# Kernel optimization log

Hardware: AMD Instinct MI355X
Metric: run time of the kernel (lower is better)

## Reference

```python
import jax, jax.numpy as jnp
import numpy as np

NUM_GRAPHS = 512

def setup_inputs() -> dict:
    key = jax.random.key(0)
    ks = jax.random.split(key, 8)
    N, E, SD = 50000, 800000, 128
    x_ids = jax.random.randint(ks[0], (N,), 0, 1340)
    edge_index = jax.random.randint(ks[1], (2, E), 0, N)
    batch = jnp.sort(jax.random.randint(ks[2], (N,), 0, NUM_GRAPHS))
    emb = jax.random.normal(ks[3], (1340, SD), dtype=jnp.float32) * 0.1
    W1 = jax.random.normal(ks[4], (SD, 2 * SD), dtype=jnp.float32) * 0.1
    b1 = jnp.zeros((2 * SD,), dtype=jnp.float32)
    W2 = jax.random.normal(ks[5], (2 * SD, 41), dtype=jnp.float32) * 0.1
    b2 = jnp.zeros((41,), dtype=jnp.float32)
    return {"x_ids": x_ids, "edge_index": edge_index, "batch": batch,
            "emb": emb, "W1": W1, "b1": b1, "W2": W2, "b2": b2}

def _gcn_conv(x, src, dst, W, b, num_nodes):
    # x: [N, Fin] -> [N, Fout]; GCN: add self-loops, deg^-1/2 norm, transform, aggregate
    deg = jax.ops.segment_sum(jnp.ones_like(dst, dtype=x.dtype), dst, num_segments=num_nodes)
    dinv = jnp.where(deg > 0, jax.lax.rsqrt(jnp.where(deg > 0, deg, 1.0)), 0.0)
    norm = dinv[src] * dinv[dst]               # [E+N]
    h = x @ W                                  # [N, Fout]
    msg = h[src] * norm[:, None]               # [E+N, Fout] gather (memory-bound)
    out = jax.ops.segment_sum(msg, dst, num_segments=num_nodes)
    return out + b

def reference(x_ids, edge_index, batch, emb, W1, b1, W2, b2):
    N = x_ids.shape[0]
    loops = jnp.arange(N, dtype=edge_index.dtype)
    src = jnp.concatenate([edge_index[0], loops])
    dst = jnp.concatenate([edge_index[1], loops])
    x = emb[x_ids]                                   # embedding lookup [N, SD]
    x = _gcn_conv(x, src, dst, W1, b1, N)
    x = jax.nn.relu(x)                               # dropout is identity in eval mode
    x = _gcn_conv(x, src, dst, W2, b2, N)
    return jax.ops.segment_sum(x, batch, num_segments=NUM_GRAPHS)  # [512, 41]
```

## Files before the change

kernel.cpp:

```cpp
#include <hip/hip_runtime.h>

#define N_NODES 50000
#define N_EDGES 800000
#define N_TOT   850000
#define SD 128
#define HD 256
#define OD 41
#define ODP 48
#define NG 512
#define NB 128
#define NPB 391
#define BCAP 8192

typedef __attribute__((ext_vector_type(8))) short bh8;
typedef __attribute__((ext_vector_type(4))) float f4;
typedef unsigned long long u64;

__device__ inline unsigned short f2bf(float x) {
  unsigned u = __float_as_uint(x);
  unsigned r = u + 0x7fff + ((u >> 16) & 1);
  return (unsigned short)(r >> 16);
}
__device__ inline float bf2f(unsigned short s) {
  return __uint_as_float(((unsigned)s) << 16);
}
__device__ inline float bflo(unsigned e) { return __uint_as_float(e << 16); }
__device__ inline float bfhi(unsigned e) { return __uint_as_float(e & 0xffff0000u); }
__device__ inline unsigned pk2(float lo, float hi) {
  return (unsigned)f2bf(lo) | ((unsigned)f2bf(hi) << 16);
}

__device__ inline unsigned rec_xid(u64 r)  { return ((unsigned)r) >> 16; }
__device__ inline unsigned rec_src(u64 r)  { return ((unsigned)r) & 0xFFFFu; }
__device__ inline float    rec_nrm(u64 r)  { return __uint_as_float((unsigned)(r >> 32) & 0xFFFF0000u); }

__global__ __launch_bounds__(256) void init_kernel(const float* __restrict__ emb,
    const float* __restrict__ W1, const float* __restrict__ W2,
    unsigned short* __restrict__ embb, unsigned short* __restrict__ w1f,
    unsigned short* __restrict__ w2f, float4* __restrict__ curB4, float4* __restrict__ out4) {
  int tid = blockIdx.x * 256 + threadIdx.x;
  if (tid < 1340 * SD) { embb[tid] = f2bf(emb[tid]); return; }
  int u = tid - 1340 * SD;
  if (u < 4096) {
    int lane = u & 63, frag = u >> 6;
    int ks = frag >> 4, cf = frag & 15;
    int col = cf * 16 + (lane & 15);
    #pragma unroll
    for (int j = 0; j < 8; ++j) {
      int k = ks * 32 + ((lane >> 4) << 3) + j;
      w1f[u * 8 + j] = f2bf(W1[k * HD + col]);
    }
    return;
  }
  u -= 4096;
  if (u < 1536) {
    int lane = u & 63, frag = u >> 6;
    int ks = frag / 3, cf = frag % 3;
    int col = cf * 16 + (lane & 15);
    #pragma unroll
    for (int j = 0; j < 8; ++j) {
      int k = ks * 32 + ((lane >> 4) << 3) + j;
      w2f[u * 8 + j] = (col < OD) ? f2bf(W2[k * OD + col]) : (unsigned short)0;
    }
    return;
  }
  u -= 1536;
  float4 z = make_float4(0.f, 0.f, 0.f, 0.f);
  if (u < 32) { curB4[u] = z; return; }
  u -= 32;
  if (u < 5248) out4[u] = z;
}

__global__ __launch_bounds__(256) void passA_kernel(const int* __restrict__ ei,
    const int* __restrict__ x_ids, int* __restrict__ curB, u64* __restrict__ stage) {
  __shared__ int lcur[NB];
  __shared__ int base[NB];
  int t = threadIdx.x;
  if (t < NB) lcur[t] = 0;
  __syncthreads();
  u64 pay[16];
  int loc[16];
  int e0 = blockIdx.x * 4096;
  #pragma unroll
  for (int j = 0; j < 16; ++j) {
    int e = e0 + j * 256 + t;
    loc[j] = -1;
    if (e < N_TOT) {
      int s, d;
      if (e < N_EDGES) { s = ei[e]; d = ei[N_EDGES + e]; }
      else             { s = d = e - N_EDGES; }
      int b = d / NPB;
      int lofs = atomicAdd(&lcur[b], 1);
      loc[j] = (b << 13) | lofs;
      pay[j] = ((u64)(unsigned)x_ids[s] << 32) | ((u64)(unsigned)d << 16) | (u64)(unsigned)s;
    }
  }
  __syncthreads();
  if (t < NB) base[t] = atomicAdd(&curB[t], lcur[t]);
  __syncthreads();
  #pragma unroll
  for (int j = 0; j < 16; ++j) {
    if (loc[j] >= 0) {
      int b = loc[j] >> 13, lofs = loc[j] & 8191;
      stage[(size_t)b * BCAP + base[b] + lofs] = pay[j];
    }
  }
}

__global__ __launch_bounds__(256) void count_kernel(const int* __restrict__ curB,
    const u64* __restrict__ stage, int* __restrict__ vcnt, float* __restrict__ dinv) {
  __shared__ int cl[NPB];
  int t = threadIdx.x, k = blockIdx.x;
  for (int l = t; l < NPB; l += 256) cl[l] = 0;
  __syncthreads();
  int nbk = curB[k];
  const u64* st = stage + (size_t)k * BCAP;
  for (int i = t; i < nbk; i += 256) {
    int d = (int)((st[i] >> 16) & 0xFFFFu);
    atomicAdd(&cl[d - k * NPB], 1);
  }
  __syncthreads();
  int n0 = k * NPB;
  int nn = (n0 + NPB <= N_NODES) ? NPB : (N_NODES - n0);
  for (int l = t; l < nn; l += 256) {
    int v = cl[l];
    vcnt[n0 + l] = v;
    dinv[n0 + l] = rsqrtf((float)v);
  }
}

__global__ __launch_bounds__(256) void scan1_kernel(const int* __restrict__ vcnt,
    int* __restrict__ off, int* __restrict__ bsum) {
  __shared__ int lds[256];
  int t = threadIdx.x;
  int i = blockIdx.x * 256 + t;
  int v = (i < N_NODES) ? vcnt[i] : 0;
  lds[t] = v;
  __syncthreads();
  for (int s = 1; s < 256; s <<= 1) {
    int add = (t >= s) ? lds[t - s] : 0;
    __syncthreads();
    lds[t] += add;
    __syncthreads();
  }
  int inc = lds[t];
  if (i < N_NODES) off[i] = inc - v;
  if (t == 255) bsum[blockIdx.x] = inc;
}

__global__ __launch_bounds__(256) void scan3g_kernel(int* __restrict__ off,
    const int* __restrict__ bsum, const int* __restrict__ batch, int* __restrict__ gstart) {
  __shared__ int lds[256];
  int t = threadIdx.x;
  int v = (t < 196) ? bsum[t] : 0;
  lds[t] = v;
  __syncthreads();
  for (int s = 1; s < 256; s <<= 1) {
    int add = (t >= s) ? lds[t - s] : 0;
    __syncthreads();
    lds[t] += add;
    __syncthreads();
  }
  int b = blockIdx.x;
  int bso = (b == 0) ? 0 : lds[b - 1];
  int i = b * 256 + t;
  if (i < N_NODES) off[i] += bso;
  if (i == 0) off[N_NODES] = N_TOT;
  if (i < N_NODES) {
    if (i == 0) {
      for (int g = 0; g <= batch[0]; ++g) gstart[g] = 0;
    } else {
      int bp = batch[i - 1], bn = batch[i];
      for (int g = bp + 1; g <= bn; ++g) gstart[g] = i;
    }
    if (i == N_NODES - 1) {
      for (int g = batch[i] + 1; g <= NG; ++g) gstart[g] = N_NODES;
    }
  }
}

__global__ __launch_bounds__(256) void passB_kernel(const int* __restrict__ curB,
    const u64* __restrict__ stage, const int* __restrict__ off,
    const float* __restrict__ dinv, u64* __restrict__ rec) {
  __shared__ int lcur[NPB];
  __shared__ int loff[NPB];
  int t = threadIdx.x, k = blockIdx.x;
  int n0 = k * NPB;
  int nn = (n0 + NPB <= N_NODES) ? NPB : (N_NODES - n0);
  for (int l = t; l < nn; l += 256) { lcur[l] = 0; loff[l] = off[n0 + l]; }
  __syncthreads();
  int nbk = curB[k];
  const u64* st = stage + (size_t)k * BCAP;
  for (int i = t; i < nbk; i += 256) {
    u64 r = st[i];
    int s   = (int)(r & 0xFFFFu);
    int d   = (int)((r >> 16) & 0xFFFFu);
    int xid = (int)((r >> 32) & 0xFFFFu);
    float nrm = dinv[s] * dinv[d];
    int ld = d - n0;
    int p = loff[ld] + atomicAdd(&lcur[ld], 1);
    rec[p] = ((u64)f2bf(nrm) << 48) | ((u64)(unsigned)xid << 16) | (u64)(unsigned)s;
  }
}

__global__ __launch_bounds__(256) void agg1w_kernel(const int* __restrict__ off,
    const u64* __restrict__ rec, const uint4* __restrict__ emb16,
    uint4* __restrict__ agg16) {
  int lane = threadIdx.x & 63;
  int node = __builtin_amdgcn_readfirstlane(blockIdx.x * 4 + (threadIdx.x >> 6));
  int beg = off[node], end = off[node + 1];
  int eslot = lane >> 4, fgrp = lane & 15;
  float a[8];
  #pragma unroll
  for (int j = 0; j < 8; ++j) a[j] = 0.f;
  int i = beg;
  for (; i + 8 <= end; i += 8) {
    u64 rA = rec[i + eslot];
    u64 rB = rec[i + 4 + eslot];
    uint4 vA = emb16[rec_xid(rA) * 16 + fgrp];
    uint4 vB = emb16[rec_xid(rB) * 16 + fgrp];
    float nA = rec_nrm(rA), nB = rec_nrm(rB);
    a[0] += nA * bflo(vA.x); a[1] += nA * bfhi(vA.x);
    a[2] += nA * bflo(vA.y); a[3] += nA * bfhi(vA.y);
    a[4] += nA * bflo(vA.z); a[5] += nA * bfhi(vA.z);
    a[6] += nA * bflo(vA.w); a[7] += nA * bfhi(vA.w);
    a[0] += nB * bflo(vB.x); a[1] += nB * bfhi(vB.x);
    a[2] += nB * bflo(vB.y); a[3] += nB * bfhi(vB.y);
    a[4] += nB * bflo(vB.z); a[5] += nB * bfhi(vB.z);
    a[6] += nB * bflo(vB.w); a[7] += nB * bfhi(vB.w);
  }
  for (; i < end; i += 4) {
    int idx = i + eslot;
    bool val = idx < end;
    u64 r = rec[val ? idx : (end - 1)];
    uint4 v = emb16[rec_xid(r) * 16 + fgrp];
    float n = val ? rec_nrm(r) : 0.f;
    a[0] += n * bflo(v.x); a[1] += n * bfhi(v.x);
    a[2] += n * bflo(v.y); a[3] += n * bfhi(v.y);
    a[4] += n * bflo(v.z); a[5] += n * bfhi(v.z);
    a[6] += n * bflo(v.w); a[7] += n * bfhi(v.w);
  }
  #pragma unroll
  for (int j = 0; j < 8; ++j) {
    a[j] += __shfl_xor(a[j], 16);
    a[j] += __shfl_xor(a[j], 32);
  }
  if (lane < 16) {
    uint4 o;
    o.x = pk2(a[0], a[1]); o.y = pk2(a[2], a[3]);
    o.z = pk2(a[4], a[5]); o.w = pk2(a[6], a[7]);
    agg16[(size_t)node * 16 + fgrp] = o;
  }
}

__global__ __launch_bounds__(256) void gemm12_mfma(const unsigned short* __restrict__ agg1,
    const bh8* __restrict__ w1f, const float* __restrict__ b1,
    const bh8* __restrict__ w2f, unsigned short* __restrict__ h2b) {
  __shared__ char raw[32768];
  int t = threadIdx.x, lane = t & 63, wave = t >> 6;
  int row0 = blockIdx.x * 64;
  #pragma unroll
  for (int k = 0; k < 4; ++k) {
    int idx = k * 256 + t;
    int r = idx >> 4, cc = idx & 15;
    int4 v = make_int4(0, 0, 0, 0);
    if (row0 + r < N_NODES)
      v = *(const int4*)((const char*)agg1 + (size_t)(row0 + r) * 256 + cc * 16);
    *(int4*)(raw + ((r * 256 + cc * 16) ^ ((r & 15) << 4))) = v;
  }
  bh8 bf1[4][4];
  #pragma unroll
  for (int cf = 0; cf < 4; ++cf)
    #pragma unroll
    for (int ks = 0; ks < 4; ++ks)
      bf1[cf][ks] = w1f[(ks * 16 + wave * 4 + cf) * 64 + lane];
  f4 acc[4][4];
  #pragma unroll
  for (int rf = 0; rf < 4; ++rf)
    #pragma unroll
    for (int cf = 0; cf < 4; ++cf)
      acc[rf][cf] = (f4){0.f, 0.f, 0.f, 0.f};
  __syncthreads();
  #pragma unroll
  for (int ks = 0; ks < 4; ++ks) {
    bh8 a[4];
    #pragma unroll
    for (int rf = 0; rf < 4; ++rf) {
      int r = rf * 16 + (lane & 15);
      int byte = (r * 256 + ks * 64 + ((lane >> 4) << 4)) ^ ((r & 15) << 4);
      a[rf] = *(const bh8*)(raw + byte);
    }
    #pragma unroll
    for (int rf = 0; rf < 4; ++rf)
      #pragma unroll
      for (int cf = 0; cf < 4; ++cf)
        acc[rf][cf] = __builtin_amdgcn_mfma_f32_16x16x32_bf16(a[rf], bf1[cf][ks], acc[rf][cf], 0, 0, 0);
  }
  __syncthreads();
  #pragma unroll
  for (int cf = 0; cf < 4; ++cf) {
    int col = wave * 64 + cf * 16 + (lane & 15);
    float bias = b1[col];
    #pragma unroll
    for (int rf = 0; rf < 4; ++rf)
      #pragma unroll
      for (int j = 0; j < 4; ++j) {
        int r = rf * 16 + ((lane >> 4) << 2) + j;
        unsigned short v = f2bf(fmaxf(acc[rf][cf][j] + bias, 0.f));
        *(unsigned short*)(raw + ((r * 512 + col * 2) ^ ((r & 15) << 4))) = v;
      }
  }
  bh8 bf2[3][8];
  #pragma unroll
  for (int cf = 0; cf < 3; ++cf)
    #pragma unroll
    for (int ks = 0; ks < 8; ++ks)
      bf2[cf][ks] = w2f[(ks * 3 + cf) * 64 + lane];
  f4 acc2[3];
  #pragma unroll
  for (int cf = 0; cf < 3; ++cf) acc2[cf] = (f4){0.f, 0.f, 0.f, 0.f};
  __syncthreads();
  int r2 = wave * 16 + (lane & 15);
  #pragma unroll
  for (int ks = 0; ks < 8; ++ks) {
    int byte = (r2 * 512 + ks * 64 + ((lane >> 4) << 4)) ^ ((r2 & 15) << 4);
    bh8 a = *(const bh8*)(raw + byte);
    #pragma unroll
    for (int cf = 0; cf < 3; ++cf)
      acc2[cf] = __builtin_amdgcn_mfma_f32_16x16x32_bf16(a, bf2[cf][ks], acc2[cf], 0, 0, 0);
  }
  #pragma unroll
  for (int cf = 0; cf < 3; ++cf) {
    int col = cf * 16 + (lane & 15);
    #pragma unroll
    for (int j = 0; j < 4; ++j) {
      int rg = row0 + wave * 16 + ((lane >> 4) << 2) + j;
      if (rg < N_NODES)
        h2b[(size_t)rg * ODP + col] = f2bf(acc2[cf][j]);
    }
  }
}

__global__ __launch_bounds__(256) void pool2_kernel(const int* __restrict__ gstart,
    const int* __restrict__ off, const u64* __restrict__ rec,
    const unsigned short* __restrict__ h2b, const float* __restrict__ b2,
    float* __restrict__ out) {
  __shared__ float red[4][60][8];
  int g = blockIdx.x >> 3, c = blockIdx.x & 7;
  int t = threadIdx.x, lane = t & 63, wv = t >> 6;
  int n0 = gstart[g], n1 = gstart[g + 1];
  int e0 = off[n0], e1 = off[n1];
  int len = e1 - e0;
  int c0 = e0 + ((len * c) >> 3);
  int c1 = e0 + ((len * (c + 1)) >> 3);
  int clen = c1 - c0;
  int w0 = c0 + ((clen * wv) >> 2);
  int w1 = c0 + ((clen * (wv + 1)) >> 2);
  bool live = lane < 60;
  int eslot = live ? lane / 6 : 0;
  int fgrp  = live ? lane - (lane / 6) * 6 : 0;
  float a[8];
  #pragma unroll
  for (int j = 0; j < 8; ++j) a[j] = 0.f;
  int i = w0;
  for (; i + 10 <= w1; i += 10) {
    u64 r = rec[i + eslot];
    uint4 v = *(const uint4*)(h2b + (size_t)rec_src(r) * ODP + fgrp * 8);
    float n = live ? rec_nrm(r) : 0.f;
    a[0] += n * bflo(v.x); a[1] += n * bfhi(v.x);
    a[2] += n * bflo(v.y); a[3] += n * bfhi(v.y);
    a[4] += n * bflo(v.z); a[5] += n * bfhi(v.z);
    a[6] += n * bflo(v.w); a[7] += n * bfhi(v.w);
  }
  if (i < w1) {
    int idx = i + eslot;
    bool val = live && idx < w1;
    u64 r = rec[val ? idx : w0];
    uint4 v = *(const uint4*)(h2b + (size_t)rec_src(r) * ODP + fgrp * 8);
    float n = val ? rec_nrm(r) : 0.f;
    a[0] += n * bflo(v.x); a[1] += n * bfhi(v.x);
    a[2] += n * bflo(v.y); a[3] += n * bfhi(v.y);
    a[4] += n * bflo(v.z); a[5] += n * bfhi(v.z);
    a[6] += n * bflo(v.w); a[7] += n * bfhi(v.w);
  }
  if (live) {
    #pragma unroll
    for (int j = 0; j < 8; ++j) red[wv][lane][j] = a[j];
  }
  __syncthreads();
  if (t < 48) {
    int fg = t >> 3, j = t & 7;
    float s = 0.f;
    #pragma unroll
    for (int w = 0; w < 4; ++w)
      #pragma unroll
      for (int e = 0; e < 10; ++e)
        s += red[w][e * 6 + fg][j];
    if (t < OD) {
      if (c == 0) s += (float)(n1 - n0) * b2[t];
      unsafeAtomicAdd(&out[g * OD + t], s);
    }
  }
}

extern "C" void kernel_launch(void* const* d_in, const int* in_sizes, int n_in,
                              void* d_out, int out_size, void* d_ws, size_t ws_size,
                              hipStream_t stream) {
  const int*   x_ids = (const int*)d_in[0];
  const int*   ei    = (const int*)d_in[1];
  const int*   batch = (const int*)d_in[2];
  const float* emb   = (const float*)d_in[3];
  const float* W1    = (const float*)d_in[4];
  const float* b1    = (const float*)d_in[5];
  const float* W2    = (const float*)d_in[6];
  const float* b2    = (const float*)d_in[7];
  float* out = (float*)d_out;
  char* ws = (char*)d_ws;

  int*            vcnt   = (int*)           (ws + 0);
  int*            curB   = (int*)           (ws + 204800);
  float*          dinv   = (float*)         (ws + 208896);
  int*            off    = (int*)           (ws + 413696);
  int*            bsum   = (int*)           (ws + 618496);
  int*            gstart = (int*)           (ws + 620544);
  unsigned short* embb   = (unsigned short*)(ws + 1048576);
  unsigned short* w1f    = (unsigned short*)(ws + 1441792);
  unsigned short* w2f    = (unsigned short*)(ws + 1507328);
  u64*            rec    = (u64*)           (ws + 2097152);
  u64*            stage  = (u64*)           (ws + 9437184);
  unsigned short* agg1   = (unsigned short*)(ws + 18874368);
  unsigned short* h2b    = (unsigned short*)(ws + 33554432);

  init_kernel <<<713, 256, 0, stream>>>(emb, W1, W2, embb, w1f, w2f,
                                        (float4*)curB, (float4*)out);
  passA_kernel<<<208, 256, 0, stream>>>(ei, x_ids, curB, stage);
  count_kernel<<<NB,  256, 0, stream>>>(curB, stage, vcnt, dinv);
  scan1_kernel<<<196, 256, 0, stream>>>(vcnt, off, bsum);
  scan3g_kernel<<<196, 256, 0, stream>>>(off, bsum, batch, gstart);
  passB_kernel<<<NB,  256, 0, stream>>>(curB, stage, off, dinv, rec);

  agg1w_kernel<<<12500, 256, 0, stream>>>(off, rec, (const uint4*)embb, (uint4*)agg1);
  gemm12_mfma <<<782,   256, 0, stream>>>(agg1, (const bh8*)w1f, b1, (const bh8*)w2f, h2b);
  pool2_kernel<<<4096,  256, 0, stream>>>(gstart, off, rec, h2b, b2, out);
}
```

Baseline: 106.0 us.

## Fuse degree count with prefix scan, move gstart into init, deepen gather unrolls

```diff
diff --git a/kernel.cpp b/kernel.cpp
--- a/kernel.cpp
+++ b/kernel.cpp
@@ -36,8 +36,10 @@
 
 __global__ __launch_bounds__(256) void init_kernel(const float* __restrict__ emb,
     const float* __restrict__ W1, const float* __restrict__ W2,
+    const int* __restrict__ batch,
     unsigned short* __restrict__ embb, unsigned short* __restrict__ w1f,
-    unsigned short* __restrict__ w2f, float4* __restrict__ curB4, float4* __restrict__ out4) {
+    unsigned short* __restrict__ w2f, float4* __restrict__ curB4,
+    float4* __restrict__ out4, int* __restrict__ gstart) {
   int tid = blockIdx.x * 256 + threadIdx.x;
   if (tid < 1340 * SD) { embb[tid] = f2bf(emb[tid]); return; }
   int u = tid - 1340 * SD;
@@ -68,7 +70,20 @@
   float4 z = make_float4(0.f, 0.f, 0.f, 0.f);
   if (u < 32) { curB4[u] = z; return; }
   u -= 32;
-  if (u < 5248) out4[u] = z;
+  if (u < 5248) { out4[u] = z; return; }
+  u -= 5248;
+  if (u < N_NODES) {
+    int i = u;
+    if (i == 0) {
+      for (int g = 0; g <= batch[0]; ++g) gstart[g] = 0;
+    } else {
+      int bp = batch[i - 1], bn = batch[i];
+      for (int g = bp + 1; g <= bn; ++g) gstart[g] = i;
+    }
+    if (i == N_NODES - 1) {
+      for (int g = batch[i] + 1; g <= NG; ++g) gstart[g] = N_NODES;
+    }
+  }
 }
 
 __global__ __launch_bounds__(256) void passA_kernel(const int* __restrict__ ei,
@@ -107,12 +122,22 @@
   }
 }
 
-__global__ __launch_bounds__(256) void count_kernel(const int* __restrict__ curB,
-    const u64* __restrict__ stage, int* __restrict__ vcnt, float* __restrict__ dinv) {
+__global__ __launch_bounds__(256) void countscan_kernel(const int* __restrict__ curB,
+    const u64* __restrict__ stage, int* __restrict__ off, float* __restrict__ dinv) {
   __shared__ int cl[NPB];
+  __shared__ int sc[512];
+  __shared__ int bs[NB];
   int t = threadIdx.x, k = blockIdx.x;
   for (int l = t; l < NPB; l += 256) cl[l] = 0;
-  __syncthreads();
+  if (t < NB) bs[t] = curB[t];
+  __syncthreads();
+  for (int s = 1; s < NB; s <<= 1) {
+    int a = (t < NB && t >= s) ? bs[t - s] : 0;
+    __syncthreads();
+    if (t < NB) bs[t] += a;
+    __syncthreads();
+  }
+  int base = (k == 0) ? 0 : bs[k - 1];
   int nbk = curB[k];
   const u64* st = stage + (size_t)k * BCAP;
   for (int i = t; i < nbk; i += 256) {
@@ -120,63 +145,24 @@
     atomicAdd(&cl[d - k * NPB], 1);
   }
   __syncthreads();
+  sc[t]       = (t < NPB)       ? cl[t]       : 0;
+  sc[t + 256] = (t + 256 < NPB) ? cl[t + 256] : 0;
+  __syncthreads();
+  for (int s = 1; s < 512; s <<= 1) {
+    int a0 = (t >= s) ? sc[t - s] : 0;
+    int a1 = (t + 256 >= s) ? sc[t + 256 - s] : 0;
+    __syncthreads();
+    sc[t] += a0; sc[t + 256] += a1;
+    __syncthreads();
+  }
   int n0 = k * NPB;
   int nn = (n0 + NPB <= N_NODES) ? NPB : (N_NODES - n0);
   for (int l = t; l < nn; l += 256) {
     int v = cl[l];
-    vcnt[n0 + l] = v;
+    off[n0 + l] = base + sc[l] - v;
     dinv[n0 + l] = rsqrtf((float)v);
   }
-}
-
-__global__ __launch_bounds__(256) void scan1_kernel(const int* __restrict__ vcnt,
-    int* __restrict__ off, int* __restrict__ bsum) {
-  __shared__ int lds[256];
-  int t = threadIdx.x;
-  int i = blockIdx.x * 256 + t;
-  int v = (i < N_NODES) ? vcnt[i] : 0;
-  lds[t] = v;
-  __syncthreads();
-  for (int s = 1; s < 256; s <<= 1) {
-    int add = (t >= s) ? lds[t - s] : 0;
-    __syncthreads();
-    lds[t] += add;
-    __syncthreads();
-  }
-  int inc = lds[t];
-  if (i < N_NODES) off[i] = inc - v;
-  if (t == 255) bsum[blockIdx.x] = inc;
-}
-
-__global__ __launch_bounds__(256) void scan3g_kernel(int* __restrict__ off,
-    const int* __restrict__ bsum, const int* __restrict__ batch, int* __restrict__ gstart) {
-  __shared__ int lds[256];
-  int t = threadIdx.x;
-  int v = (t < 196) ? bsum[t] : 0;
-  lds[t] = v;
-  __syncthreads();
-  for (int s = 1; s < 256; s <<= 1) {
-    int add = (t >= s) ? lds[t - s] : 0;
-    __syncthreads();
-    lds[t] += add;
-    __syncthreads();
-  }
-  int b = blockIdx.x;
-  int bso = (b == 0) ? 0 : lds[b - 1];
-  int i = b * 256 + t;
-  if (i < N_NODES) off[i] += bso;
-  if (i == 0) off[N_NODES] = N_TOT;
-  if (i < N_NODES) {
-    if (i == 0) {
-      for (int g = 0; g <= batch[0]; ++g) gstart[g] = 0;
-    } else {
-      int bp = batch[i - 1], bn = batch[i];
-      for (int g = bp + 1; g <= bn; ++g) gstart[g] = i;
-    }
-    if (i == N_NODES - 1) {
-      for (int g = batch[i] + 1; g <= NG; ++g) gstart[g] = N_NODES;
-    }
-  }
+  if (k == 0 && t == 0) off[N_NODES] = N_TOT;
 }
 
 __global__ __launch_bounds__(256) void passB_kernel(const int* __restrict__ curB,
@@ -214,6 +200,33 @@
   #pragma unroll
   for (int j = 0; j < 8; ++j) a[j] = 0.f;
   int i = beg;
+  for (; i + 16 <= end; i += 16) {
+    u64 r0 = rec[i + eslot];
+    u64 r1 = rec[i + 4 + eslot];
+    u64 r2 = rec[i + 8 + eslot];
+    u64 r3 = rec[i + 12 + eslot];
+    uint4 v0 = emb16[rec_xid(r0) * 16 + fgrp];
+    uint4 v1 = emb16[rec_xid(r1) * 16 + fgrp];
+    uint4 v2 = emb16[rec_xid(r2) * 16 + fgrp];
+    uint4 v3 = emb16[rec_xid(r3) * 16 + fgrp];
+    float n0 = rec_nrm(r0), n1 = rec_nrm(r1), n2 = rec_nrm(r2), n3 = rec_nrm(r3);
+    a[0] += n0 * bflo(v0.x); a[1] += n0 * bfhi(v0.x);
+    a[2] += n0 * bflo(v0.y); a[3] += n0 * bfhi(v0.y);
+    a[4] += n0 * bflo(v0.z); a[5] += n0 * bfhi(v0.z);
+    a[6] += n0 * bflo(v0.w); a[7] += n0 * bfhi(v0.w);
+    a[0] += n1 * bflo(v1.x); a[1] += n1 * bfhi(v1.x);
+    a[2] += n1 * bflo(v1.y); a[3] += n1 * bfhi(v1.y);
+    a[4] += n1 * bflo(v1.z); a[5] += n1 * bfhi(v1.z);
+    a[6] += n1 * bflo(v1.w); a[7] += n1 * bfhi(v1.w);
+    a[0] += n2 * bflo(v2.x); a[1] += n2 * bfhi(v2.x);
+    a[2] += n2 * bflo(v2.y); a[3] += n2 * bfhi(v2.y);
+    a[4] += n2 * bflo(v2.z); a[5] += n2 * bfhi(v2.z);
+    a[6] += n2 * bflo(v2.w); a[7] += n2 * bfhi(v2.w);
+    a[0] += n3 * bflo(v3.x); a[1] += n3 * bfhi(v3.x);
+    a[2] += n3 * bflo(v3.y); a[3] += n3 * bfhi(v3.y);
+    a[4] += n3 * bflo(v3.z); a[5] += n3 * bfhi(v3.z);
+    a[6] += n3 * bflo(v3.w); a[7] += n3 * bfhi(v3.w);
+  }
   for (; i + 8 <= end; i += 8) {
     u64 rA = rec[i + eslot];
     u64 rB = rec[i + 4 + eslot];
@@ -363,6 +376,22 @@
   #pragma unroll
   for (int j = 0; j < 8; ++j) a[j] = 0.f;
   int i = w0;
+  for (; i + 20 <= w1; i += 20) {
+    u64 rA = rec[i + eslot];
+    u64 rB = rec[i + 10 + eslot];
+    uint4 vA = *(const uint4*)(h2b + (size_t)rec_src(rA) * ODP + fgrp * 8);
+    uint4 vB = *(const uint4*)(h2b + (size_t)rec_src(rB) * ODP + fgrp * 8);
+    float nA = live ? rec_nrm(rA) : 0.f;
+    float nB = live ? rec_nrm(rB) : 0.f;
+    a[0] += nA * bflo(vA.x); a[1] += nA * bfhi(vA.x);
+    a[2] += nA * bflo(vA.y); a[3] += nA * bfhi(vA.y);
+    a[4] += nA * bflo(vA.z); a[5] += nA * bfhi(vA.z);
+    a[6] += nA * bflo(vA.w); a[7] += nA * bfhi(vA.w);
+    a[0] += nB * bflo(vB.x); a[1] += nB * bfhi(vB.x);
+    a[2] += nB * bflo(vB.y); a[3] += nB * bfhi(vB.y);
+    a[4] += nB * bflo(vB.z); a[5] += nB * bfhi(vB.z);
+    a[6] += nB * bflo(vB.w); a[7] += nB * bfhi(vB.w);
+  }
   for (; i + 10 <= w1; i += 10) {
     u64 r = rec[i + eslot];
     uint4 v = *(const uint4*)(h2b + (size_t)rec_src(r) * ODP + fgrp * 8);
@@ -417,12 +446,10 @@
   float* out = (float*)d_out;
   char* ws = (char*)d_ws;
 
-  int*            vcnt   = (int*)           (ws + 0);
-  int*            curB   = (int*)           (ws + 204800);
-  float*          dinv   = (float*)         (ws + 208896);
-  int*            off    = (int*)           (ws + 413696);
-  int*            bsum   = (int*)           (ws + 618496);
-  int*            gstart = (int*)           (ws + 620544);
+  int*            curB   = (int*)           (ws + 0);
+  float*          dinv   = (float*)         (ws + 4096);
+  int*            off    = (int*)           (ws + 208896);
+  int*            gstart = (int*)           (ws + 413696);
   unsigned short* embb   = (unsigned short*)(ws + 1048576);
   unsigned short* w1f    = (unsigned short*)(ws + 1441792);
   unsigned short* w2f    = (unsigned short*)(ws + 1507328);
@@ -431,12 +458,10 @@
   unsigned short* agg1   = (unsigned short*)(ws + 18874368);
   unsigned short* h2b    = (unsigned short*)(ws + 33554432);
 
-  init_kernel <<<713, 256, 0, stream>>>(emb, W1, W2, embb, w1f, w2f,
-                                        (float4*)curB, (float4*)out);
+  init_kernel <<<908, 256, 0, stream>>>(emb, W1, W2, batch, embb, w1f, w2f,
+                                        (float4*)curB, (float4*)out, gstart);
   passA_kernel<<<208, 256, 0, stream>>>(ei, x_ids, curB, stage);
-  count_kernel<<<NB,  256, 0, stream>>>(curB, stage, vcnt, dinv);
-  scan1_kernel<<<196, 256, 0, stream>>>(vcnt, off, bsum);
-  scan3g_kernel<<<196, 256, 0, stream>>>(off, bsum, batch, gstart);
+  countscan_kernel<<<NB, 256, 0, stream>>>(curB, stage, off, dinv);
   passB_kernel<<<NB,  256, 0, stream>>>(curB, stage, off, dinv, rec);
 
   agg1w_kernel<<<12500, 256, 0, stream>>>(off, rec, (const uint4*)embb, (uint4*)agg1);
```

Result: faster. 101.8 us (-3.9%).
